# Performance work log

Hardware: AMD Instinct MI355X
Metric: run time of the kernel (lower is better)

The kernel has to match this reference:

```python
import jax, jax.numpy as jnp
import numpy as np

SEARCH_SIZE = 21
BLOCK_SIZE = 4


def _inter_prediction(im1, im2, search_size=SEARCH_SIZE, block_size=BLOCK_SIZE):
    # im1, im2: [B, 1, H, W]; returns [B, 1, H, W]
    B, C, H, W = im1.shape
    p = search_size // 2
    s2 = search_size * search_size
    im2_pad = jnp.pad(im2, ((0, 0), (0, 0), (p, p), (p, p)))
    # All SxS shifted views of im2, stacked on channel dim: [B, S^2, H, W].
    # Channel k = (i, j) row-major corresponds to im2_pad[:, :, i:i+H, j:j+W],
    # matching the torch double loop (note: output is permutation-invariant
    # over shifts anyway since weights are derived from the same tensor).
    nbr = jax.lax.conv_general_dilated_patches(
        im2_pad, (search_size, search_size), (1, 1), 'VALID')
    diff = jnp.abs(im1 - nbr)  # broadcast [B,1,H,W] against [B,S^2,H,W]
    h, w = H // block_size, W // block_size
    # avg_pool2d with kernel=stride=block_size via reshape-mean
    vol = diff.reshape(B, s2, h, block_size, w, block_size).mean(axis=(3, 5))
    idx = jax.nn.softmax(-100.0 * vol, axis=1)  # [B, S^2, h, w]
    # repeat_interleave(block_size) along both spatial dims
    idx_full = jnp.broadcast_to(
        idx[:, :, :, None, :, None],
        (B, s2, h, block_size, w, block_size)).reshape(B, s2, H, W)
    return jnp.sum(idx_full * nbr, axis=1, keepdims=True)


def setup_inputs() -> dict:
    key = jax.random.key(0)
    k1, k2 = jax.random.split(key)
    im1 = jax.random.normal(k1, (2, 1, 256, 256), dtype=jnp.float32)
    im2 = jax.random.normal(k2, (2, 1, 256, 256), dtype=jnp.float32)
    return {"im1": im1, "im2": im2}


def reference(im1, im2):
    return _inter_prediction(im1, im2)
```

## Files before the change

### kernel.cpp

```cpp
#include <hip/hip_runtime.h>
#include <math.h>


typedef float v2f __attribute__((ext_vector_type(2)));

#define HH 256
#define WW 256
#define PAD 10
#define NR 28
#define NC 28
#define CSTR 30
#define COPY (NC * CSTR)
#define LDSN (2 * COPY)

__global__ __launch_bounds__(256) void pred_kernel(
    const float* __restrict__ im1, const float* __restrict__ im2,
    float* __restrict__ out) {
  __shared__ __attribute__((aligned(16))) float win2[LDSN];

  const int tid = threadIdx.x;
  const int T = blockIdx.x;
  const int b = T >> 10;
  const int rem = T & 1023;
  const int tr = rem >> 5;
  const int tc = rem & 31;
  const float* im2b = im2 + b * (HH * WW);

  for (int e = tid; e < NR * NC; e += 256) {
    const int r = e / NC;
    const int c = e - r * NC;
    const int gr = tr * 8 + r - PAD;
    const int gc = tc * 8 + c - PAD;
    float v = 0.f;
    if ((unsigned)gr < HH && (unsigned)gc < WW) v = im2b[gr * WW + gc];
    win2[c * CSTR + r] = v;
    if (r >= 1) win2[COPY + c * CSTR + (r - 1)] = v;
  }
  __syncthreads();

  const int wave = tid >> 6;
  const int lane = tid & 63;
  const int by = tr * 2 + (wave >> 1);
  const int bx = tc * 2 + (wave & 1);

  v2f a2[4][2];
  {
    const float* im1b = im1 + b * (HH * WW) + (by * 4) * WW + bx * 4;
    const float4 r0 = *reinterpret_cast<const float4*>(im1b + 0 * WW);
    const float4 r1 = *reinterpret_cast<const float4*>(im1b + 1 * WW);
    const float4 r2 = *reinterpret_cast<const float4*>(im1b + 2 * WW);
    const float4 r3 = *reinterpret_cast<const float4*>(im1b + 3 * WW);
    a2[0][0] = (v2f){r0.x, r1.x}; a2[1][0] = (v2f){r0.y, r1.y};
    a2[2][0] = (v2f){r0.z, r1.z}; a2[3][0] = (v2f){r0.w, r1.w};
    a2[0][1] = (v2f){r2.x, r3.x}; a2[1][1] = (v2f){r2.y, r3.y};
    a2[2][1] = (v2f){r2.z, r3.z}; a2[3][1] = (v2f){r2.w, r3.w};
  }

  const int i = lane / 3;
  const int j0 = (lane - i * 3) * 7;
  const int ir = i + (wave >> 1) * 4;
  const int jc = j0 + (wave & 1) * 4;
  const int par = ir & 1;
  const int q0 = ir - par;
  const int baseIdx = par * COPY + jc * CSTR + q0;

  v2f w2[10][2];
#pragma unroll
  for (int c = 0; c < 10; ++c) {
#pragma unroll
    for (int rp = 0; rp < 2; ++rp)
      w2[c][rp] = *reinterpret_cast<const v2f*>(
          &win2[baseIdx + c * CSTR + 2 * rp]);
  }

  float sad[7];
#pragma unroll
  for (int t = 0; t < 7; ++t) {
    v2f acc = (v2f){0.f, 0.f};
#pragma unroll
    for (int c = 0; c < 4; ++c) {
#pragma unroll
      for (int rp = 0; rp < 2; ++rp) {
        const v2f d = a2[c][rp] - w2[t + c][rp];
        acc += __builtin_elementwise_max(d, -d);
      }
    }
    sad[t] = acc.x + acc.y;
  }
  if (lane == 63) {
#pragma unroll
    for (int t = 0; t < 7; ++t) sad[t] = 3.0e38f;
  }

  float m = sad[0];
#pragma unroll
  for (int t = 1; t < 7; ++t) m = fminf(m, sad[t]);
#pragma unroll
  for (int off = 32; off; off >>= 1) m = fminf(m, __shfl_xor(m, off, 64));

  const float cc = 9.016844005556021f;
  const float cm = cc * m;
  float l = 0.f;
  v2f o2[4][2];
#pragma unroll
  for (int c = 0; c < 4; ++c)
#pragma unroll
    for (int rp = 0; rp < 2; ++rp) o2[c][rp] = (v2f){0.f, 0.f};
#pragma unroll
  for (int t = 0; t < 7; ++t) {
    const float p = __builtin_amdgcn_exp2f(__builtin_fmaf(-cc, sad[t], cm));
    l += p;
    const v2f pv = (v2f){p, p};
#pragma unroll
    for (int c = 0; c < 4; ++c)
#pragma unroll
      for (int rp = 0; rp < 2; ++rp)
        o2[c][rp] += pv * w2[t + c][rp];
  }

  float o[16];
#pragma unroll
  for (int c = 0; c < 4; ++c)
#pragma unroll
    for (int rp = 0; rp < 2; ++rp) {
      o[(2 * rp + 0) * 4 + c] = o2[c][rp].x;
      o[(2 * rp + 1) * 4 + c] = o2[c][rp].y;
    }

  float r8[8];
  {
    const bool up = (lane & 32) != 0;
#pragma unroll
    for (int q = 0; q < 8; ++q) {
      const float send = up ? o[q] : o[q + 8];
      const float recv = __shfl_xor(send, 32, 64);
      r8[q] = (up ? o[q + 8] : o[q]) + recv;
    }
  }
  float r4[4];
  {
    const bool up = (lane & 16) != 0;
#pragma unroll
    for (int q = 0; q < 4; ++q) {
      const float send = up ? r8[q] : r8[q + 4];
      const float recv = __shfl_xor(send, 16, 64);
      r4[q] = (up ? r8[q + 4] : r8[q]) + recv;
    }
  }
  float r2[2];
  {
    const bool up = (lane & 8) != 0;
#pragma unroll
    for (int q = 0; q < 2; ++q) {
      const float send = up ? r4[q] : r4[q + 2];
      const float recv = __shfl_xor(send, 8, 64);
      r2[q] = (up ? r4[q + 2] : r4[q]) + recv;
    }
  }
  float r1;
  {
    const bool up = (lane & 4) != 0;
    const float send = up ? r2[0] : r2[1];
    const float recv = __shfl_xor(send, 4, 64);
    r1 = (up ? r2[1] : r2[0]) + recv;
  }
  r1 += __shfl_xor(r1, 2, 64);
  r1 += __shfl_xor(r1, 1, 64);

#pragma unroll
  for (int off = 32; off; off >>= 1) l += __shfl_xor(l, off, 64);
  const float rinv = __builtin_amdgcn_rcpf(l);

  if ((lane & 3) == 0) {
    const int t = lane >> 2;
    out[b * (HH * WW) + (by * 4 + (t >> 2)) * WW + bx * 4 + (t & 3)] =
        r1 * rinv;
  }
}

extern "C" void kernel_launch(void* const* d_in, const int* in_sizes, int n_in,
                              void* d_out, int out_size, void* d_ws, size_t ws_size,
                              hipStream_t stream) {
  const float* im1 = (const float*)d_in[0];
  const float* im2 = (const float*)d_in[1];
  float* out = (float*)d_out;
  const int B = in_sizes[0] / (HH * WW);
  pred_kernel<<<B * 1024, 256, 0, stream>>>(im1, im2, out);
}
```

Baseline: 64.06 us.

## Use single-copy LDS window with float2 global loads and interior fast path

Drops the duplicated parity-shifted LDS copy and uses one column-major window with stride 29, so each lane reads LDS as scalars instead of aligned 8-byte pairs. The global-to-LDS fill now loads float2 pairs, with a branch-free path for interior tiles and bounds checks only for border tiles. The im1 load is moved ahead of the fill, and launch bounds now request four blocks per SM. This halves LDS footprint and fill stores but doubles the LDS read instruction count in the compute phase.

```diff
diff --git a/kernel.cpp b/kernel.cpp
--- a/kernel.cpp
+++ b/kernel.cpp
@@ -9,11 +9,10 @@
 #define PAD 10
 #define NR 28
 #define NC 28
-#define CSTR 30
-#define COPY (NC * CSTR)
-#define LDSN (2 * COPY)
-
-__global__ __launch_bounds__(256) void pred_kernel(
+#define CSTR 29
+#define LDSN (NC * CSTR)
+
+__global__ __launch_bounds__(256, 4) void pred_kernel(
     const float* __restrict__ im1, const float* __restrict__ im2,
     float* __restrict__ out) {
   __shared__ __attribute__((aligned(16))) float win2[LDSN];
@@ -25,18 +24,6 @@
   const int tr = rem >> 5;
   const int tc = rem & 31;
   const float* im2b = im2 + b * (HH * WW);
-
-  for (int e = tid; e < NR * NC; e += 256) {
-    const int r = e / NC;
-    const int c = e - r * NC;
-    const int gr = tr * 8 + r - PAD;
-    const int gc = tc * 8 + c - PAD;
-    float v = 0.f;
-    if ((unsigned)gr < HH && (unsigned)gc < WW) v = im2b[gr * WW + gc];
-    win2[c * CSTR + r] = v;
-    if (r >= 1) win2[COPY + c * CSTR + (r - 1)] = v;
-  }
-  __syncthreads();
 
   const int wave = tid >> 6;
   const int lane = tid & 63;
@@ -56,21 +43,46 @@
     a2[2][1] = (v2f){r2.z, r3.z}; a2[3][1] = (v2f){r2.w, r3.w};
   }
 
+  {
+    const int gr0 = tr * 8 - PAD;
+    const int gc0 = tc * 8 - PAD;
+    if (((unsigned)(tr - 2) < 28u) & ((unsigned)(tc - 2) < 28u)) {
+      for (int e = tid; e < NR * (NC / 2); e += 256) {
+        const int r = e / 14;
+        const int c2 = e - r * 14;
+        const float2 v = *reinterpret_cast<const float2*>(
+            &im2b[(gr0 + r) * WW + (gc0 + 2 * c2)]);
+        win2[(2 * c2 + 0) * CSTR + r] = v.x;
+        win2[(2 * c2 + 1) * CSTR + r] = v.y;
+      }
+    } else {
+      for (int e = tid; e < NR * (NC / 2); e += 256) {
+        const int r = e / 14;
+        const int c2 = e - r * 14;
+        const int gr = gr0 + r;
+        const int gc = gc0 + 2 * c2;
+        float2 v = {0.f, 0.f};
+        if (((unsigned)gr < HH) & ((unsigned)gc < WW))
+          v = *reinterpret_cast<const float2*>(&im2b[gr * WW + gc]);
+        win2[(2 * c2 + 0) * CSTR + r] = v.x;
+        win2[(2 * c2 + 1) * CSTR + r] = v.y;
+      }
+    }
+  }
+  __syncthreads();
+
   const int i = lane / 3;
   const int j0 = (lane - i * 3) * 7;
   const int ir = i + (wave >> 1) * 4;
   const int jc = j0 + (wave & 1) * 4;
-  const int par = ir & 1;
-  const int q0 = ir - par;
-  const int baseIdx = par * COPY + jc * CSTR + q0;
+  const int baseIdx = (lane == 63) ? 0 : (jc * CSTR + ir);
 
   v2f w2[10][2];
 #pragma unroll
   for (int c = 0; c < 10; ++c) {
-#pragma unroll
-    for (int rp = 0; rp < 2; ++rp)
-      w2[c][rp] = *reinterpret_cast<const v2f*>(
-          &win2[baseIdx + c * CSTR + 2 * rp]);
+    const float* p = &win2[baseIdx + c * CSTR];
+    w2[c][0] = (v2f){p[0], p[1]};
+    w2[c][1] = (v2f){p[2], p[3]};
   }
 
   float sad[7];
```

Result: no change. 63.15 us (-1.4%).
